# Performance work log

Hardware: AMD Instinct MI355X
Metric: run time of the kernel (lower is better)

Reference implementation:

```python
import jax, jax.numpy as jnp
import numpy as np
from jax import lax

# Straight-through sign: forward sign(x), backward passes grad where |x|<=1 (hardtanh STE)
@jax.custom_vjp
def sign_ste(x):
    return jnp.sign(x)

def _sign_fwd(x):
    return jnp.sign(x), x

def _sign_bwd(x, g):
    return (g * (jnp.abs(x) <= 1.0).astype(g.dtype),)

sign_ste.defvjp(_sign_fwd, _sign_bwd)

STRIDE = 1
PADDING = 1

def setup_inputs() -> dict:
    key = jax.random.key(0)
    k1, k2, k3 = jax.random.split(key, 3)
    B, Cin, H, W = 32, 256, 56, 56
    Cout, K = 256, 3
    inp = jax.random.normal(k1, (B, Cin, H, W), dtype=jnp.float32)
    # kaiming-uniform-ish init like torch Conv2d default
    fan_in = Cin * K * K
    bound = 1.0 / np.sqrt(fan_in)
    weight1 = jax.random.uniform(k2, (Cout, Cin, K, K), minval=-bound, maxval=bound, dtype=jnp.float32)
    weight2 = jax.random.uniform(k3, (Cout, Cin, K, K), minval=-bound, maxval=bound, dtype=jnp.float32)
    return {"input": inp, "weight1": weight1, "weight2": weight2}

def reference(input, weight1, weight2):
    # ternarized weight: (sign(w1)+sign(w2))/2 in {-1,-0.5,0,0.5,1}
    w_ter = (sign_ste(weight1) + sign_ste(weight2)) * 0.5
    x_bin = sign_ste(input)
    out = lax.conv_general_dilated(
        x_bin, w_ter,
        window_strides=(STRIDE, STRIDE),
        padding=[(PADDING, PADDING), (PADDING, PADDING)],
        dimension_numbers=("NCHW", "OIHW", "NCHW"),
    )
    # per-output-channel scaling: mean|w1| + mean|w2| over (in, kh, kw)
    alpha = jnp.mean(jnp.abs(weight1), axis=(1, 2, 3)) + jnp.mean(jnp.abs(weight2), axis=(1, 2, 3))
    return out * alpha[None, :, None, None]
```

## Files before the change

### kernel.cpp

```cpp
#include <hip/hip_runtime.h>
#include <hip/hip_bf16.h>

#define B_    32
#define C_    256
#define H_    56
#define W_    56
#define HP    58
#define WPAD  58
#define HW    3136
#define CHW   802816
#define M_TOT 100352

typedef char charx16 __attribute__((ext_vector_type(16)));
typedef int  intx4   __attribute__((ext_vector_type(4)));

#define XPAD_BYTES (B_ * HP * WPAD * C_)
#define WPK_BYTES  (C_ * 9 * C_)

__global__ __launch_bounds__(256) void pack_w_kernel(const float* __restrict__ w1,
                                                     const float* __restrict__ w2,
                                                     char* __restrict__ wq,
                                                     float* __restrict__ alphah) {
  const int co = blockIdx.x;
  const int ci = threadIdx.x;
  const int base = (co * C_ + ci) * 9;
  float sabs = 0.f;
#pragma unroll
  for (int s = 0; s < 9; ++s) {
    const float a = w1[base + s];
    const float b = w2[base + s];
    const int sa = (a > 0.f) - (a < 0.f);
    const int sb = (b > 0.f) - (b < 0.f);
    wq[(co * 9 + s) * C_ + ci] = (char)(sa + sb);
    sabs += fabsf(a) + fabsf(b);
  }
#pragma unroll
  for (int off = 32; off > 0; off >>= 1) sabs += __shfl_down(sabs, off, 64);
  __shared__ float red[4];
  if ((threadIdx.x & 63) == 0) red[threadIdx.x >> 6] = sabs;
  __syncthreads();
  if (threadIdx.x == 0)
    alphah[co] = (red[0] + red[1] + red[2] + red[3]) * (0.5f / 2304.0f);
}

#define ROWPC 272
__global__ __launch_bounds__(256) void pack_x_kernel(const float* __restrict__ in,
                                                     char* __restrict__ xp) {
  __shared__ char row[58 * ROWPC];
  const int yp = blockIdx.x % HP;
  const int b  = blockIdx.x / HP;
  const int tid = threadIdx.x;

  float4* rz = (float4*)row;
  const float4 z4 = make_float4(0.f, 0.f, 0.f, 0.f);
#pragma unroll
  for (int i = 0; i < 4; ++i) {
    const int idx = i * 256 + tid;
    if (idx < (58 * ROWPC) / 16) rz[idx] = z4;
  }
  __syncthreads();

  const int y = yp - 1;
  const int x = tid & 63;
  const int cig = tid >> 6;
  if (y >= 0 && y < H_ && x < W_) {
    const float* src = in + ((size_t)(b * C_) * H_ + y) * W_ + x;
#pragma unroll
    for (int it = 0; it < 4; ++it) {
      const int ci0 = it * 64 + cig * 16;
      charx16 v;
#pragma unroll
      for (int j = 0; j < 16; ++j) {
        const float f = src[(size_t)(ci0 + j) * HW];
        v[j] = (char)((f > 0.f) - (f < 0.f));
      }
      *(charx16*)&row[(x + 1) * ROWPC + ci0] = v;
    }
  }
  __syncthreads();

  const int cc = tid & 15;
  const int xo = tid >> 4;
  char* dst = xp + (size_t)(b * HP + yp) * WPAD * C_;
#pragma unroll
  for (int it = 0; it < 4; ++it) {
    const int xs = it * 16 + xo;
    if (xs < WPAD)
      *(float4*)(dst + xs * C_ + cc * 16) = *(const float4*)&row[xs * ROWPC + cc * 16];
  }
}

__global__ __launch_bounds__(256, 3) void gemm_kernel(const char* __restrict__ xp,
                                                      const char* __restrict__ wq,
                                                      const float* __restrict__ alphah,
                                                      float* __restrict__ out) {
  __shared__ char sA[128 * 128];
  __shared__ char sB[128 * 128];
  const int tid = threadIdx.x;

  const int id = blockIdx.x;
  const int xcd = id & 7;
  const int l = id >> 3;
  const int co0 = (l & 1) * 128;
  const int m0 = ((l >> 1) * 8 + xcd) * 128;

  const int srow = tid >> 3;
  const int scol = (tid & 7) ^ (srow & 7);

  const char* wsrc[4];
  const char* xsrc[4];
#pragma unroll
  for (int i = 0; i < 4; ++i) {
    const int m = m0 + srow + 32 * i;
    const int b = m / HW;
    const int rem = m - b * HW;
    const int y = rem / W_;
    const int x = rem - y * W_;
    xsrc[i] = xp + ((b * HP + y) * WPAD + x) * C_ + scol * 16;
    wsrc[i] = wq + (co0 + srow + 32 * i) * 9 * C_ + scol * 16;
  }

  intx4 acc[4][4] = {};

  const int lane = tid & 63;
  const int wave = tid >> 6;
  const int wm = wave >> 1;
  const int wn = wave & 1;
  const int lrow = lane & 15;
  const int quad = lane >> 4;
  const int swk = lrow & 7;
  const int abase = (wm * 64 + lrow) * 128;
  const int bbase = (wn * 64 + lrow) * 128;

  for (int s = 0; s < 9; ++s) {
    const int woff = s * C_;
    const int shoff = ((s / 3) * WPAD + (s % 3)) * C_;
#pragma unroll
    for (int h = 0; h < 2; ++h) {
      const int hh = h * 128;
      __syncthreads();
#pragma unroll
      for (int i = 0; i < 4; ++i) {
        __builtin_amdgcn_global_load_lds(
            (const __attribute__((address_space(1))) void*)(wsrc[i] + woff + hh),
            (__attribute__((address_space(3))) void*)(sA + i * 4096 + tid * 16),
            16, 0, 0);
      }
#pragma unroll
      for (int i = 0; i < 4; ++i) {
        __builtin_amdgcn_global_load_lds(
            (const __attribute__((address_space(1))) void*)(xsrc[i] + shoff + hh),
            (__attribute__((address_space(3))) void*)(sB + i * 4096 + tid * 16),
            16, 0, 0);
      }
      __syncthreads();
#pragma unroll
      for (int kf = 0; kf < 2; ++kf) {
        const int coff = (((kf << 2) + quad) ^ swk) << 4;
        intx4 af[4], bfv[4];
#pragma unroll
        for (int i = 0; i < 4; ++i)
          af[i] = *(const intx4*)(sA + abase + i * 2048 + coff);
#pragma unroll
        for (int j = 0; j < 4; ++j)
          bfv[j] = *(const intx4*)(sB + bbase + j * 2048 + coff);
#pragma unroll
        for (int i = 0; i < 4; ++i)
#pragma unroll
          for (int j = 0; j < 4; ++j)
            acc[i][j] = __builtin_amdgcn_mfma_i32_16x16x64_i8(af[i], bfv[j],
                                                              acc[i][j], 0, 0, 0);
      }
    }
  }

  int ob[4];
#pragma unroll
  for (int j = 0; j < 4; ++j) {
    const int m = m0 + wn * 64 + j * 16 + lrow;
    const int b = m / HW;
    const int rem = m - b * HW;
    const int y = rem / W_;
    const int x = rem - y * W_;
    ob[j] = b * CHW + y * W_ + x;
  }
#pragma unroll
  for (int i = 0; i < 4; ++i) {
#pragma unroll
    for (int r = 0; r < 4; ++r) {
      const int co = co0 + wm * 64 + i * 16 + quad * 4 + r;
      const float sc = alphah[co];
#pragma unroll
      for (int j = 0; j < 4; ++j)
        out[ob[j] + co * HW] = (float)acc[i][j][r] * sc;
    }
  }
}

extern "C" void kernel_launch(void* const* d_in, const int* in_sizes, int n_in,
                              void* d_out, int out_size, void* d_ws, size_t ws_size,
                              hipStream_t stream) {
  const float* input = (const float*)d_in[0];
  const float* w1 = (const float*)d_in[1];
  const float* w2 = (const float*)d_in[2];
  float* out = (float*)d_out;

  char* ws = (char*)d_ws;
  char* xp = ws;
  char* wq = ws + XPAD_BYTES;
  float* alphah = (float*)(ws + XPAD_BYTES + WPK_BYTES);

  pack_w_kernel<<<C_, 256, 0, stream>>>(w1, w2, wq, alphah);
  pack_x_kernel<<<B_ * HP, 256, 0, stream>>>(input, xp);
  gemm_kernel<<<M_TOT / 128 * (C_ / 128), 256, 0, stream>>>(xp, wq, alphah, out);
}
```

Before: 251.6 us.

## Double-buffer LDS tiles in int8 GEMM and vectorize input/weight packing

The GEMM main loop now uses two LDS buffers for A and B, so the asynchronous global-to-LDS loads for the next K-slice are issued while MFMAs run on the current one. This removes one barrier per step and hides load latency, but it doubles LDS use per block and lowers the occupancy hint from 3 to 2. The input packing kernel now reads float4 vectors across width and packs four channel signs per 32-bit store. The weight packing kernel stages each output channel's weights in shared memory so its global reads are coalesced.

Measured after the change: 248.6 us. About the same (-1.2%).

```diff
diff --git a/kernel.cpp b/kernel.cpp
--- a/kernel.cpp
+++ b/kernel.cpp
@@ -11,24 +11,37 @@
 #define CHW   802816
 #define M_TOT 100352
 
-typedef char charx16 __attribute__((ext_vector_type(16)));
-typedef int  intx4   __attribute__((ext_vector_type(4)));
+typedef char  charx16 __attribute__((ext_vector_type(16)));
+typedef int   intx4   __attribute__((ext_vector_type(4)));
 
 #define XPAD_BYTES (B_ * HP * WPAD * C_)
 #define WPK_BYTES  (C_ * 9 * C_)
+
+__device__ __forceinline__ int sgn8(float f) {
+  return ((f > 0.f) ? 1 : ((f < 0.f) ? -1 : 0)) & 0xff;
+}
 
 __global__ __launch_bounds__(256) void pack_w_kernel(const float* __restrict__ w1,
                                                      const float* __restrict__ w2,
                                                      char* __restrict__ wq,
                                                      float* __restrict__ alphah) {
+  __shared__ float l1[2304], l2[2304];
   const int co = blockIdx.x;
-  const int ci = threadIdx.x;
-  const int base = (co * C_ + ci) * 9;
+  const int tid = threadIdx.x;
+  const float* s1 = w1 + co * 2304;
+  const float* s2 = w2 + co * 2304;
+#pragma unroll
+  for (int i = 0; i < 9; ++i) {
+    l1[i * 256 + tid] = s1[i * 256 + tid];
+    l2[i * 256 + tid] = s2[i * 256 + tid];
+  }
+  __syncthreads();
+  const int ci = tid;
   float sabs = 0.f;
 #pragma unroll
   for (int s = 0; s < 9; ++s) {
-    const float a = w1[base + s];
-    const float b = w2[base + s];
+    const float a = l1[ci * 9 + s];
+    const float b = l2[ci * 9 + s];
     const int sa = (a > 0.f) - (a < 0.f);
     const int sb = (b > 0.f) - (b < 0.f);
     wq[(co * 9 + s) * C_ + ci] = (char)(sa + sb);
@@ -37,9 +50,9 @@
 #pragma unroll
   for (int off = 32; off > 0; off >>= 1) sabs += __shfl_down(sabs, off, 64);
   __shared__ float red[4];
-  if ((threadIdx.x & 63) == 0) red[threadIdx.x >> 6] = sabs;
-  __syncthreads();
-  if (threadIdx.x == 0)
+  if ((tid & 63) == 0) red[tid >> 6] = sabs;
+  __syncthreads();
+  if (tid == 0)
     alphah[co] = (red[0] + red[1] + red[2] + red[3]) * (0.5f / 2304.0f);
 }
 
@@ -61,20 +74,29 @@
   __syncthreads();
 
   const int y = yp - 1;
-  const int x = tid & 63;
-  const int cig = tid >> 6;
-  if (y >= 0 && y < H_ && x < W_) {
-    const float* src = in + ((size_t)(b * C_) * H_ + y) * W_ + x;
-#pragma unroll
-    for (int it = 0; it < 4; ++it) {
-      const int ci0 = it * 64 + cig * 16;
-      charx16 v;
-#pragma unroll
-      for (int j = 0; j < 16; ++j) {
-        const float f = src[(size_t)(ci0 + j) * HW];
-        v[j] = (char)((f > 0.f) - (f < 0.f));
+  const int xq = tid % 14;
+  const int cs = tid / 14;
+  if (y >= 0 && y < H_ && cs < 18) {
+    const float* base = in + ((size_t)b * C_ * H_ + (size_t)y) * W_ + xq * 4;
+#pragma unroll
+    for (int k = 0; k < 4; ++k) {
+      const int cq = cs + 18 * k;
+      if (cq < 64) {
+        float4 f[4];
+#pragma unroll
+        for (int j = 0; j < 4; ++j)
+          f[j] = *(const float4*)(base + (size_t)(cq * 4 + j) * (H_ * W_));
+#pragma unroll
+        for (int d = 0; d < 4; ++d) {
+          const float v0 = (d == 0) ? f[0].x : (d == 1) ? f[0].y : (d == 2) ? f[0].z : f[0].w;
+          const float v1 = (d == 0) ? f[1].x : (d == 1) ? f[1].y : (d == 2) ? f[1].z : f[1].w;
+          const float v2 = (d == 0) ? f[2].x : (d == 1) ? f[2].y : (d == 2) ? f[2].z : f[2].w;
+          const float v3 = (d == 0) ? f[3].x : (d == 1) ? f[3].y : (d == 2) ? f[3].z : f[3].w;
+          const unsigned int pk = (unsigned)sgn8(v0) | ((unsigned)sgn8(v1) << 8) |
+                                  ((unsigned)sgn8(v2) << 16) | ((unsigned)sgn8(v3) << 24);
+          *(unsigned int*)&row[(xq * 4 + d + 1) * ROWPC + cq * 4] = pk;
+        }
       }
-      *(charx16*)&row[(x + 1) * ROWPC + ci0] = v;
     }
   }
   __syncthreads();
@@ -90,12 +112,12 @@
   }
 }
 
-__global__ __launch_bounds__(256, 3) void gemm_kernel(const char* __restrict__ xp,
+__global__ __launch_bounds__(256, 2) void gemm_kernel(const char* __restrict__ xp,
                                                       const char* __restrict__ wq,
                                                       const float* __restrict__ alphah,
                                                       float* __restrict__ out) {
-  __shared__ char sA[128 * 128];
-  __shared__ char sB[128 * 128];
+  __shared__ char sA[2 * 128 * 128];
+  __shared__ char sB[2 * 128 * 128];
   const int tid = threadIdx.x;
 
   const int id = blockIdx.x;
@@ -132,45 +154,47 @@
   const int abase = (wm * 64 + lrow) * 128;
   const int bbase = (wn * 64 + lrow) * 128;
 
-  for (int s = 0; s < 9; ++s) {
-    const int woff = s * C_;
-    const int shoff = ((s / 3) * WPAD + (s % 3)) * C_;
-#pragma unroll
-    for (int h = 0; h < 2; ++h) {
-      const int hh = h * 128;
-      __syncthreads();
-#pragma unroll
-      for (int i = 0; i < 4; ++i) {
-        __builtin_amdgcn_global_load_lds(
-            (const __attribute__((address_space(1))) void*)(wsrc[i] + woff + hh),
-            (__attribute__((address_space(3))) void*)(sA + i * 4096 + tid * 16),
-            16, 0, 0);
-      }
-#pragma unroll
-      for (int i = 0; i < 4; ++i) {
-        __builtin_amdgcn_global_load_lds(
-            (const __attribute__((address_space(1))) void*)(xsrc[i] + shoff + hh),
-            (__attribute__((address_space(3))) void*)(sB + i * 4096 + tid * 16),
-            16, 0, 0);
-      }
-      __syncthreads();
-#pragma unroll
-      for (int kf = 0; kf < 2; ++kf) {
-        const int coff = (((kf << 2) + quad) ^ swk) << 4;
-        intx4 af[4], bfv[4];
-#pragma unroll
-        for (int i = 0; i < 4; ++i)
-          af[i] = *(const intx4*)(sA + abase + i * 2048 + coff);
+  auto stage = [&](int t) {
+    const int s = t >> 1;
+    const int hh = (t & 1) * 128;
+    const int woff = s * C_ + hh;
+    const int shoff = ((s / 3) * WPAD + (s % 3)) * C_ + hh;
+    char* dA = sA + (t & 1) * 16384 + tid * 16;
+    char* dB = sB + (t & 1) * 16384 + tid * 16;
+#pragma unroll
+    for (int i = 0; i < 4; ++i)
+      __builtin_amdgcn_global_load_lds(
+          (const __attribute__((address_space(1))) void*)(wsrc[i] + woff),
+          (__attribute__((address_space(3))) void*)(dA + i * 4096), 16, 0, 0);
+#pragma unroll
+    for (int i = 0; i < 4; ++i)
+      __builtin_amdgcn_global_load_lds(
+          (const __attribute__((address_space(1))) void*)(xsrc[i] + shoff),
+          (__attribute__((address_space(3))) void*)(dB + i * 4096), 16, 0, 0);
+  };
+
+  stage(0);
+  for (int t = 0; t < 18; ++t) {
+    __syncthreads();
+    if (t < 17) stage(t + 1);
+    const char* bA = sA + (t & 1) * 16384;
+    const char* bB = sB + (t & 1) * 16384;
+#pragma unroll
+    for (int kf = 0; kf < 2; ++kf) {
+      const int coff = (((kf << 2) + quad) ^ swk) << 4;
+      intx4 af[4], bfv[4];
+#pragma unroll
+      for (int i = 0; i < 4; ++i)
+        af[i] = *(const intx4*)(bA + abase + i * 2048 + coff);
+#pragma unroll
+      for (int j = 0; j < 4; ++j)
+        bfv[j] = *(const intx4*)(bB + bbase + j * 2048 + coff);
+#pragma unroll
+      for (int i = 0; i < 4; ++i)
 #pragma unroll
         for (int j = 0; j < 4; ++j)
-          bfv[j] = *(const intx4*)(sB + bbase + j * 2048 + coff);
-#pragma unroll
-        for (int i = 0; i < 4; ++i)
-#pragma unroll
-          for (int j = 0; j < 4; ++j)
-            acc[i][j] = __builtin_amdgcn_mfma_i32_16x16x64_i8(af[i], bfv[j],
-                                                              acc[i][j], 0, 0, 0);
-      }
+          acc[i][j] = __builtin_amdgcn_mfma_i32_16x16x64_i8(af[i], bfv[j],
+                                                            acc[i][j], 0, 0, 0);
     }
   }
 
```
